# Optimization experiments

Measured on AMD Instinct MI355X. Metric: run time of the kernel, lower is better.

Reference implementation:

```python
import jax, jax.numpy as jnp
import numpy as np

B, S, H = 2, 2048, 2048
NH, KVH, HD = 16, 4, 128
R = 16
LORA_SCALE = 32.0 / 16.0  # lora_alpha / lora_r
ATTN_SCALE = HD ** -0.5
NEG = -1e9


def setup_inputs() -> dict:
    key = jax.random.key(0)
    ks = jax.random.split(key, 16)
    q_dim, kv_dim = NH * HD, KVH * HD
    # RoPE tables
    inv_freq = 1.0 / (10000.0 ** (jnp.arange(0, HD, 2, dtype=jnp.float32) / HD))
    ang = jnp.arange(S, dtype=jnp.float32)[:, None] * inv_freq[None, :]  # [S, HD/2]
    emb = jnp.concatenate([ang, ang], axis=-1)  # [S, HD]
    cos = jnp.broadcast_to(jnp.cos(emb)[None], (B, S, HD))
    sin = jnp.broadcast_to(jnp.sin(emb)[None], (B, S, HD))
    # additive causal mask [B,1,S,S]
    causal = jnp.triu(jnp.full((S, S), NEG, dtype=jnp.float32), k=1)
    attention_mask = jnp.broadcast_to(causal[None, None], (B, 1, S, S))
    return {
        'hidden_states': jax.random.normal(ks[0], (B, S, H), jnp.float32),
        'cos': cos,
        'sin': sin,
        'attention_mask': attention_mask,
        'q_w': jax.random.normal(ks[1], (q_dim, H), jnp.float32) * 0.02,
        'k_w': jax.random.normal(ks[2], (kv_dim, H), jnp.float32) * 0.02,
        'v_w': jax.random.normal(ks[3], (kv_dim, H), jnp.float32) * 0.02,
        'q_b': jax.random.normal(ks[4], (q_dim,), jnp.float32) * 0.02,
        'k_b': jax.random.normal(ks[5], (kv_dim,), jnp.float32) * 0.02,
        'v_b': jax.random.normal(ks[6], (kv_dim,), jnp.float32) * 0.02,
        'q_A': jax.random.normal(ks[7], (H, R), jnp.float32) * (1.0 / np.sqrt(H)),
        'q_B': jax.random.normal(ks[8], (R, q_dim), jnp.float32) * 0.02,
        'k_A': jax.random.normal(ks[9], (H, R), jnp.float32) * (1.0 / np.sqrt(H)),
        'k_B': jax.random.normal(ks[10], (R, kv_dim), jnp.float32) * 0.02,
        'v_A': jax.random.normal(ks[11], (H, R), jnp.float32) * (1.0 / np.sqrt(H)),
        'v_B': jax.random.normal(ks[12], (R, kv_dim), jnp.float32) * 0.02,
        'o_w': jax.random.normal(ks[13], (H, H), jnp.float32) * 0.02,
    }


def _rotate_half(x):
    x1, x2 = x[..., : HD // 2], x[..., HD // 2:]
    return jnp.concatenate([-x2, x1], axis=-1)


def reference(hidden_states, cos, sin, attention_mask,
              q_w, k_w, v_w, q_b, k_b, v_b,
              q_A, q_B, k_A, k_B, v_A, v_B, o_w):
    x = hidden_states  # dropout p=0 (eval)
    # fused base + LoRA projections
    q = x @ q_w.T + q_b + LORA_SCALE * ((x @ q_A) @ q_B)  # [B,S,NH*HD]
    k = x @ k_w.T + k_b + LORA_SCALE * ((x @ k_A) @ k_B)  # [B,S,KVH*HD]
    v = x @ v_w.T + v_b + LORA_SCALE * ((x @ v_A) @ v_B)
    q = q.reshape(B, S, NH, HD).transpose(0, 2, 1, 3)   # [B,NH,S,HD]
    k = k.reshape(B, S, KVH, HD).transpose(0, 2, 1, 3)  # [B,KVH,S,HD]
    v = v.reshape(B, S, KVH, HD).transpose(0, 2, 1, 3)
    # RoPE
    c = cos[:, None]  # [B,1,S,HD]
    s = sin[:, None]
    q = q * c + _rotate_half(q) * s
    k = k * c + _rotate_half(k) * s
    # GQA: repeat kv heads
    n_rep = NH // KVH
    k = jnp.repeat(k, n_rep, axis=1)  # [B,NH,S,HD]
    v = jnp.repeat(v, n_rep, axis=1)
    scores = jnp.einsum('bhqd,bhkd->bhqk', q, k) * ATTN_SCALE
    scores = scores + attention_mask
    attn = jax.nn.softmax(scores.astype(jnp.float32), axis=-1).astype(q.dtype)
    out = jnp.einsum('bhqk,bhkd->bhqd', attn, v)
    out = out.transpose(0, 2, 1, 3).reshape(B, S, NH * HD)  # [B,S,H]
    return out @ o_w.T
```

## Files before the change

### kernel.cpp

```cpp
#include <hip/hip_runtime.h>

constexpr int cB   = 2;
constexpr int cS   = 2048;
constexpr int cH   = 2048;
constexpr int cNH  = 16;
constexpr int cKVH = 4;
constexpr int cHD  = 128;
constexpr int cQD  = 2048;
constexpr int cKVD = 512;
constexpr int cNQKV = 3072;
constexpr int cNTOK = 4096;
#define ATTN_SCALE 0.08838834764831845f

typedef __bf16 bf16;
typedef __attribute__((ext_vector_type(8))) __bf16 bf16x8;
typedef __attribute__((ext_vector_type(4))) __bf16 bf16x4;
typedef __attribute__((ext_vector_type(4))) float  f32x4;

__device__ __forceinline__ void async_load16(const bf16* g, bf16* l) {
    __builtin_amdgcn_global_load_lds(
        (const __attribute__((address_space(1))) void*)g,
        (__attribute__((address_space(3))) void*)l, 16, 0, 0);
}

__global__ void conv_f32_bf16(const float* __restrict__ in, bf16* __restrict__ out) {
    int i = (blockIdx.x * 256 + threadIdx.x) * 4;
    f32x4 v = *(const f32x4*)(in + i);
    bf16x4 o;
    o[0] = (bf16)v[0]; o[1] = (bf16)v[1]; o[2] = (bf16)v[2]; o[3] = (bf16)v[3];
    *(bf16x4*)(out + i) = o;
}

__global__ void prep_w(const float* __restrict__ qw, const float* __restrict__ kw, const float* __restrict__ vw,
                       const float* __restrict__ qA, const float* __restrict__ qB,
                       const float* __restrict__ kA, const float* __restrict__ kB,
                       const float* __restrict__ vA, const float* __restrict__ vB,
                       bf16* __restrict__ Wc) {
    const int idx = blockIdx.x * 256 + threadIdx.x;
    const int n = idx >> 11, k = idx & 2047;
    const float* W; const float* Am; const float* Bm; int nn, nd;
    if (n < cQD)             { W = qw; Am = qA; Bm = qB; nn = n;          nd = cQD; }
    else if (n < cQD + cKVD) { W = kw; Am = kA; Bm = kB; nn = n - cQD;    nd = cKVD; }
    else                     { W = vw; Am = vA; Bm = vB; nn = n - cQD - cKVD; nd = cKVD; }
    float acc = 0.f;
    #pragma unroll
    for (int r = 0; r < 16; ++r) acc += Am[k * 16 + r] * Bm[r * nd + nn];
    Wc[(size_t)n * cH + k] = (bf16)(W[(size_t)nn * cH + k] + 2.0f * acc);
}

__global__ void prep_bias(const float* __restrict__ qb, const float* __restrict__ kb,
                          const float* __restrict__ vb, float* __restrict__ biasc) {
    int n = blockIdx.x * 256 + threadIdx.x;
    if (n >= cNQKV) return;
    biasc[n] = (n < cQD) ? qb[n] : (n < cQD + cKVD ? kb[n - cQD] : vb[n - cQD - cKVD]);
}

__global__ __launch_bounds__(256) void gemm_qkv(const bf16* __restrict__ A, const bf16* __restrict__ Bw,
                                                const float* __restrict__ bias,
                                                const float* __restrict__ cosb, const float* __restrict__ sinb,
                                                bf16* __restrict__ Qr, bf16* __restrict__ Kr,
                                                bf16* __restrict__ Vt) {
    __shared__ bf16 Al[128 * 32];
    __shared__ bf16 Bl[128 * 32];
    const int tid = threadIdx.x;
    const int wave = tid >> 6, lane = tid & 63;
    const int quad = lane >> 4, l16 = lane & 15;
    const int wr = wave >> 1, wc = wave & 1;
    const long bm = (long)blockIdx.y * 128, bn = (long)blockIdx.x * 128;
    const int K = cH;

    f32x4 acc[4][4];
    #pragma unroll
    for (int i = 0; i < 4; ++i)
        #pragma unroll
        for (int c = 0; c < 4; ++c) acc[i][c] = f32x4{0.f, 0.f, 0.f, 0.f};

    const int r0 = lane >> 2;
    const int kc = (lane & 3) * 8;

    for (int k0 = 0; k0 < K; k0 += 32) {
        __syncthreads();
        #pragma unroll
        for (int j = 0; j < 2; ++j) {
            const int rb = (wave * 2 + j) * 16;
            const int row = rb + r0;
            async_load16(A  + (size_t)(bm + row) * K + k0 + kc, &Al[rb * 32 + r0 * 32 + kc]);
            async_load16(Bw + (size_t)(bn + row) * K + k0 + kc, &Bl[rb * 32 + r0 * 32 + kc]);
        }
        __syncthreads();
        bf16x8 af[4], bfr[4];
        #pragma unroll
        for (int i = 0; i < 4; ++i) af[i]  = *(const bf16x8*)&Al[(wr * 64 + i * 16 + l16) * 32 + quad * 8];
        #pragma unroll
        for (int c = 0; c < 4; ++c) {
            const int nrow = wc * 32 + (c & 1) * 16 + (c >> 1) * 64 + l16;
            bfr[c] = *(const bf16x8*)&Bl[nrow * 32 + quad * 8];
        }
        #pragma unroll
        for (int i = 0; i < 4; ++i)
            #pragma unroll
            for (int c = 0; c < 4; ++c)
                acc[i][c] = __builtin_amdgcn_mfma_f32_16x16x32_bf16(af[i], bfr[c], acc[i][c], 0, 0, 0);
    }

    #pragma unroll
    for (int c = 0; c < 4; ++c) {
        const int nloc = wc * 32 + (c & 1) * 16 + (c >> 1) * 64 + l16;
        const float bv = bias[bn + nloc];
        #pragma unroll
        for (int i = 0; i < 4; ++i)
            #pragma unroll
            for (int r = 0; r < 4; ++r) acc[i][c][r] += bv;
    }

    const int head = (int)(bn >> 7);
    if (head < cNH + cKVH) {
        const bool isQ = head < cNH;
        #pragma unroll
        for (int cl = 0; cl < 2; ++cl) {
            const int d = wc * 32 + cl * 16 + l16;
            #pragma unroll
            for (int i = 0; i < 4; ++i)
                #pragma unroll
                for (int r = 0; r < 4; ++r) {
                    const long t = bm + wr * 64 + i * 16 + quad * 4 + r;
                    const float cv = cosb[t * cHD + d];
                    const float sv = sinb[t * cHD + d];
                    const float v1 = acc[i][cl][r], v2 = acc[i][cl + 2][r];
                    float o1 = v1 * cv - v2 * sv;
                    float o2 = v2 * cv + v1 * sv;
                    if (isQ) { o1 *= ATTN_SCALE; o2 *= ATTN_SCALE; }
                    const int b = (int)(t >> 11), s = (int)(t & 2047);
                    bf16* dst = isQ
                        ? Qr + ((size_t)(b * cNH + head) * cS + s) * cHD
                        : Kr + ((size_t)(b * cKVH + (head - cNH)) * cS + s) * cHD;
                    dst[d]      = (bf16)o1;
                    dst[d + 64] = (bf16)o2;
                }
        }
    } else {
        const int kv = head - cNH - cKVH;
        const int b = (int)(bm >> 11);
        const int sbase = (int)(bm & 2047);
        #pragma unroll
        for (int c = 0; c < 4; ++c) {
            const int d = wc * 32 + (c & 1) * 16 + (c >> 1) * 64 + l16;
            #pragma unroll
            for (int i = 0; i < 4; ++i) {
                const int s0 = sbase + wr * 64 + i * 16 + quad * 4;
                bf16x4 o4;
                #pragma unroll
                for (int r = 0; r < 4; ++r) o4[r] = (bf16)acc[i][c][r];
                *(bf16x4*)&Vt[((size_t)((b * cKVH + kv) * cHD) + d) * cS + s0] = o4;
            }
        }
    }
}

__global__ __launch_bounds__(256) void gemm_bt_f32(const bf16* __restrict__ A, const bf16* __restrict__ Bw,
                                                   float* __restrict__ Cp, int M, int N, int K) {
    __shared__ bf16 Al[128 * 32];
    __shared__ bf16 Bl[128 * 32];
    const int tid = threadIdx.x;
    const int wave = tid >> 6, lane = tid & 63;
    const int quad = lane >> 4, l16 = lane & 15;
    const int wr = wave >> 1, wc = wave & 1;
    const long bm = (long)blockIdx.y * 128, bn = (long)blockIdx.x * 128;

    f32x4 acc[4][4];
    #pragma unroll
    for (int i = 0; i < 4; ++i)
        #pragma unroll
        for (int c = 0; c < 4; ++c) acc[i][c] = f32x4{0.f, 0.f, 0.f, 0.f};

    const int r0 = lane >> 2;
    const int kc = (lane & 3) * 8;

    for (int k0 = 0; k0 < K; k0 += 32) {
        __syncthreads();
        #pragma unroll
        for (int j = 0; j < 2; ++j) {
            const int rb = (wave * 2 + j) * 16;
            const int row = rb + r0;
            async_load16(A  + (size_t)(bm + row) * K + k0 + kc, &Al[rb * 32 + r0 * 32 + kc]);
            async_load16(Bw + (size_t)(bn + row) * K + k0 + kc, &Bl[rb * 32 + r0 * 32 + kc]);
        }
        __syncthreads();
        bf16x8 af[4], bfr[4];
        #pragma unroll
        for (int i = 0; i < 4; ++i) af[i]  = *(const bf16x8*)&Al[(wr * 64 + i * 16 + l16) * 32 + quad * 8];
        #pragma unroll
        for (int c = 0; c < 4; ++c) bfr[c] = *(const bf16x8*)&Bl[(wc * 64 + c * 16 + l16) * 32 + quad * 8];
        #pragma unroll
        for (int i = 0; i < 4; ++i)
            #pragma unroll
            for (int c = 0; c < 4; ++c)
                acc[i][c] = __builtin_amdgcn_mfma_f32_16x16x32_bf16(af[i], bfr[c], acc[i][c], 0, 0, 0);
    }

    #pragma unroll
    for (int i = 0; i < 4; ++i)
        #pragma unroll
        for (int c = 0; c < 4; ++c) {
            const long m0 = bm + wr * 64 + i * 16 + quad * 4;
            const long n  = bn + wc * 64 + c * 16 + l16;
            #pragma unroll
            for (int r = 0; r < 4; ++r)
                Cp[(m0 + r) * N + n] = acc[i][c][r];
        }
}

__global__ __launch_bounds__(256, 2) void flash4(const bf16* __restrict__ Q, const bf16* __restrict__ K,
                                                 const bf16* __restrict__ Vt, bf16* __restrict__ Ob) {
    __shared__ bf16 kb[8192];
    __shared__ bf16 vb[8192];
    __shared__ bf16 pb[4096];
    const int tid = threadIdx.x;
    const int wave = tid >> 6, lane = tid & 63;
    const int quad = lane >> 4, l16 = lane & 15;
    const int pi = blockIdx.x;
    const int h = blockIdx.y, b = blockIdx.z;

    const bf16* Qh = Q  + (size_t)(b * cNH + h) * cS * cHD;
    const bf16* Kg = K  + (size_t)(b * cKVH + (h >> 2)) * cS * cHD;
    const bf16* Vg = Vt + (size_t)(b * cKVH + (h >> 2)) * cHD * cS;

    int kgo[4], vgo[4], slo[4];
    #pragma unroll
    for (int i2 = 0; i2 < 4; ++i2) {
        const int si = i2 * 256 + tid;
        const int krow = si >> 4, kcsw = si & 15;
        const int kc = (kcsw & 8) | ((kcsw & 7) ^ (krow & 7));
        kgo[i2] = krow * cHD + kc * 8;
        const int vrow = si >> 3, vcsw = si & 7;
        const int vc = vcsw ^ (vrow & 7);
        vgo[i2] = vrow * cS + vc * 8;
        slo[i2] = si * 8;
    }

    #pragma unroll
    for (int t2 = 0; t2 < 2; ++t2) {
        const int qt = t2 == 0 ? (31 - pi) : pi;

        const bf16* Qg = Qh + (size_t)qt * 64 * cHD;
        bf16x8 qf[4];
        #pragma unroll
        for (int ks = 0; ks < 4; ++ks)
            qf[ks] = *(const bf16x8*)(Qg + (size_t)(wave * 16 + l16) * cHD + ks * 32 + quad * 8);

        f32x4 oac[8];
        #pragma unroll
        for (int dt = 0; dt < 8; ++dt) oac[dt] = f32x4{0.f, 0.f, 0.f, 0.f};
        float m_ = -3.0e38f, l_ = 0.f;

        const int nkt = qt + 1;
        for (int kt = 0; kt < nkt; ++kt) {
            __syncthreads();
            const bf16* Kt  = Kg + (size_t)kt * 64 * cHD;
            const bf16* Vtt = Vg + kt * 64;
            #pragma unroll
            for (int i2 = 0; i2 < 4; ++i2) async_load16(Kt + kgo[i2], kb + slo[i2]);
            #pragma unroll
            for (int i2 = 0; i2 < 4; ++i2) async_load16(Vtt + vgo[i2], vb + slo[i2]);
            __syncthreads();

            f32x4 st[4];
            #pragma unroll
            for (int mt = 0; mt < 4; ++mt) {
                bf16x8 kf[4];
                #pragma unroll
                for (int ks = 0; ks < 4; ++ks) {
                    const int c = ks * 4 + quad;
                    const int csw = (c & 8) | ((c & 7) ^ (l16 & 7));
                    kf[ks] = *(const bf16x8*)&kb[(mt * 16 + l16) * 128 + csw * 8];
                }
                f32x4 a = f32x4{0.f, 0.f, 0.f, 0.f};
                #pragma unroll
                for (int ks = 0; ks < 4; ++ks)
                    a = __builtin_amdgcn_mfma_f32_16x16x32_bf16(kf[ks], qf[ks], a, 0, 0, 0);
                st[mt] = a;
            }

            const int qpos = qt * 64 + wave * 16 + l16;
            const bool dm = (kt * 64 + 63) > (qt * 64 + wave * 16);
            float tmax = -3.0e38f;
            #pragma unroll
            for (int mt = 0; mt < 4; ++mt)
                #pragma unroll
                for (int r = 0; r < 4; ++r) {
                    float v = st[mt][r];
                    if (dm) {
                        const int kpos = kt * 64 + mt * 16 + quad * 4 + r;
                        if (kpos > qpos) v = -3.0e38f;
                    }
                    st[mt][r] = v;
                    tmax = fmaxf(tmax, v);
                }
            tmax = fmaxf(tmax, __shfl_xor(tmax, 16, 64));
            tmax = fmaxf(tmax, __shfl_xor(tmax, 32, 64));
            const float mnew = fmaxf(m_, tmax);
            const float alpha = __expf(m_ - mnew);
            m_ = mnew;
            float rs = 0.f;
            #pragma unroll
            for (int mt = 0; mt < 4; ++mt)
                #pragma unroll
                for (int r = 0; r < 4; ++r) {
                    const float p = __expf(st[mt][r] - mnew);
                    st[mt][r] = p;
                    rs += p;
                }
            rs += __shfl_xor(rs, 16, 64);
            rs += __shfl_xor(rs, 32, 64);
            l_ = l_ * alpha + rs;
            #pragma unroll
            for (int dt = 0; dt < 8; ++dt)
                #pragma unroll
                for (int r = 0; r < 4; ++r) oac[dt][r] *= alpha;

            #pragma unroll
            for (int mt = 0; mt < 4; ++mt) {
                bf16x4 p4;
                #pragma unroll
                for (int r = 0; r < 4; ++r) p4[r] = (bf16)st[mt][r];
                const int csw = (mt * 2 + (quad >> 1)) ^ (l16 & 7);
                *(bf16x4*)&pb[wave * 1024 + l16 * 64 + csw * 8 + (quad & 1) * 4] = p4;
            }

            bf16x8 pf[2];
            #pragma unroll
            for (int ks = 0; ks < 2; ++ks) {
                const int c = ks * 4 + quad;
                const int csw = c ^ (l16 & 7);
                pf[ks] = *(const bf16x8*)&pb[wave * 1024 + l16 * 64 + csw * 8];
            }
            #pragma unroll
            for (int dt = 0; dt < 8; ++dt) {
                bf16x8 vf[2];
                #pragma unroll
                for (int ks = 0; ks < 2; ++ks) {
                    const int c = ks * 4 + quad;
                    const int csw = c ^ (l16 & 7);
                    vf[ks] = *(const bf16x8*)&vb[(dt * 16 + l16) * 64 + csw * 8];
                }
                #pragma unroll
                for (int ks = 0; ks < 2; ++ks)
                    oac[dt] = __builtin_amdgcn_mfma_f32_16x16x32_bf16(vf[ks], pf[ks], oac[dt], 0, 0, 0);
            }
        }

        const float inv = 1.0f / l_;
        const int token = qt * 64 + wave * 16 + l16;
        bf16* orow = Ob + (size_t)(b * cS + token) * (cNH * cHD) + h * cHD;
        #pragma unroll
        for (int dt = 0; dt < 8; ++dt) {
            bf16x4 o4;
            #pragma unroll
            for (int r = 0; r < 4; ++r) o4[r] = (bf16)(oac[dt][r] * inv);
            *(bf16x4*)&orow[dt * 16 + quad * 4] = o4;
        }
    }
}

extern "C" void kernel_launch(void* const* d_in, const int* in_sizes, int n_in,
                              void* d_out, int out_size, void* d_ws, size_t ws_size,
                              hipStream_t stream) {
    const float* x    = (const float*)d_in[0];
    const float* cosb = (const float*)d_in[1];
    const float* sinb = (const float*)d_in[2];
    const float* qw = (const float*)d_in[4];
    const float* kw = (const float*)d_in[5];
    const float* vw = (const float*)d_in[6];
    const float* qb = (const float*)d_in[7];
    const float* kb_ = (const float*)d_in[8];
    const float* vb = (const float*)d_in[9];
    const float* qA = (const float*)d_in[10];
    const float* qB = (const float*)d_in[11];
    const float* kA = (const float*)d_in[12];
    const float* kB = (const float*)d_in[13];
    const float* vA = (const float*)d_in[14];
    const float* vB = (const float*)d_in[15];
    const float* ow = (const float*)d_in[16];
    float* out = (float*)d_out;

    char* ws = (char*)d_ws;
    bf16* Xbf   = (bf16*)ws;  ws += (size_t)cNTOK * cH * 2;
    bf16* Wc    = (bf16*)ws;  ws += (size_t)cNQKV * cH * 2;
    float* biasc = (float*)ws; ws += (size_t)cNQKV * 4;
    bf16* Qr    = (bf16*)ws;  ws += (size_t)cB * cNH * cS * cHD * 2;
    bf16* Kr    = (bf16*)ws;  ws += (size_t)cB * cKVH * cS * cHD * 2;
    bf16* Vt    = (bf16*)ws;  ws += (size_t)cB * cKVH * cHD * cS * 2;
    bf16* OWbf  = (bf16*)ws;  ws += (size_t)cH * cH * 2;
    bf16* Aout  = (bf16*)ws;  ws += (size_t)cNTOK * cQD * 2;

    conv_f32_bf16<<<(cNTOK * cH) / 1024, 256, 0, stream>>>(x, Xbf);
    conv_f32_bf16<<<(cH * cH) / 1024, 256, 0, stream>>>(ow, OWbf);
    prep_w<<<(cNQKV * cH) / 256, 256, 0, stream>>>(qw, kw, vw, qA, qB, kA, kB, vA, vB, Wc);
    prep_bias<<<(cNQKV + 255) / 256, 256, 0, stream>>>(qb, kb_, vb, biasc);

    gemm_qkv<<<dim3(cNQKV / 128, cNTOK / 128), 256, 0, stream>>>(Xbf, Wc, biasc, cosb, sinb, Qr, Kr, Vt);

    flash4<<<dim3(16, cNH, cB), 256, 0, stream>>>(Qr, Kr, Vt, Aout);

    gemm_bt_f32<<<dim3(cH / 128, cNTOK / 128), 256, 0, stream>>>(Aout, OWbf, out, cNTOK, cH, cH);
}
```

Measured before the change: 406.8 us.

## Widen GEMM K-tile with swizzled LDS, vectorize weight prep, use exp2 in flash softmax

Both GEMMs now stage 64-wide K tiles into LDS with an XOR swizzle, which halves the number of loop iterations and barriers and avoids LDS bank conflicts. Weight prep is rewritten to handle 8 contiguous K elements per thread with vector loads, and the bias-prep kernel is folded into it. The flash kernel folds log2(e) into the Q scale so softmax can use exp2. It also skips the accumulator rescale when no row max increases and splits the masked and unmasked max paths. Doubling LDS per block may lower occupancy.

```diff
diff --git a/kernel.cpp b/kernel.cpp
--- a/kernel.cpp
+++ b/kernel.cpp
@@ -11,6 +11,7 @@
 constexpr int cNQKV = 3072;
 constexpr int cNTOK = 4096;
 #define ATTN_SCALE 0.08838834764831845f
+#define QSCALE 0.12751589549581288f
 
 typedef __bf16 bf16;
 typedef __attribute__((ext_vector_type(8))) __bf16 bf16x8;
@@ -31,28 +32,40 @@
     *(bf16x4*)(out + i) = o;
 }
 
-__global__ void prep_w(const float* __restrict__ qw, const float* __restrict__ kw, const float* __restrict__ vw,
-                       const float* __restrict__ qA, const float* __restrict__ qB,
-                       const float* __restrict__ kA, const float* __restrict__ kB,
-                       const float* __restrict__ vA, const float* __restrict__ vB,
-                       bf16* __restrict__ Wc) {
-    const int idx = blockIdx.x * 256 + threadIdx.x;
-    const int n = idx >> 11, k = idx & 2047;
-    const float* W; const float* Am; const float* Bm; int nn, nd;
-    if (n < cQD)             { W = qw; Am = qA; Bm = qB; nn = n;          nd = cQD; }
-    else if (n < cQD + cKVD) { W = kw; Am = kA; Bm = kB; nn = n - cQD;    nd = cKVD; }
-    else                     { W = vw; Am = vA; Bm = vB; nn = n - cQD - cKVD; nd = cKVD; }
-    float acc = 0.f;
-    #pragma unroll
-    for (int r = 0; r < 16; ++r) acc += Am[k * 16 + r] * Bm[r * nd + nn];
-    Wc[(size_t)n * cH + k] = (bf16)(W[(size_t)nn * cH + k] + 2.0f * acc);
-}
-
-__global__ void prep_bias(const float* __restrict__ qb, const float* __restrict__ kb,
-                          const float* __restrict__ vb, float* __restrict__ biasc) {
-    int n = blockIdx.x * 256 + threadIdx.x;
-    if (n >= cNQKV) return;
-    biasc[n] = (n < cQD) ? qb[n] : (n < cQD + cKVD ? kb[n - cQD] : vb[n - cQD - cKVD]);
+__global__ __launch_bounds__(256) void prep_w2(
+        const float* __restrict__ qw, const float* __restrict__ kw, const float* __restrict__ vw,
+        const float* __restrict__ qA, const float* __restrict__ qB,
+        const float* __restrict__ kA, const float* __restrict__ kB,
+        const float* __restrict__ vA, const float* __restrict__ vB,
+        const float* __restrict__ qb, const float* __restrict__ kbias, const float* __restrict__ vb,
+        bf16* __restrict__ Wc, float* __restrict__ biasc) {
+    const int wave = threadIdx.x >> 6, lane = threadIdx.x & 63;
+    const int n = blockIdx.y * 4 + wave;
+    const int k0 = blockIdx.x * 512 + lane * 8;
+    const float* W; const float* Am; const float* Bm; const float* bias; int nn, nd;
+    if (n < cQD)             { W = qw; Am = qA; Bm = qB; bias = qb;    nn = n;               nd = cQD; }
+    else if (n < cQD + cKVD) { W = kw; Am = kA; Bm = kB; bias = kbias; nn = n - cQD;         nd = cKVD; }
+    else                     { W = vw; Am = vA; Bm = vB; bias = vb;    nn = n - cQD - cKVD;  nd = cKVD; }
+    if (blockIdx.x == 0 && lane == 0) biasc[n] = bias[nn];
+    float bm[16];
+    #pragma unroll
+    for (int r = 0; r < 16; ++r) bm[r] = Bm[r * nd + nn];
+    const float* wrow = W + (size_t)nn * cH + k0;
+    f32x4 w0 = *(const f32x4*)(wrow);
+    f32x4 w1 = *(const f32x4*)(wrow + 4);
+    bf16x8 o;
+    #pragma unroll
+    for (int j = 0; j < 8; ++j) {
+        const f32x4* am = (const f32x4*)(Am + (size_t)(k0 + j) * 16);
+        f32x4 a0 = am[0], a1 = am[1], a2 = am[2], a3 = am[3];
+        float acc = 0.f;
+        #pragma unroll
+        for (int c = 0; c < 4; ++c) acc += a0[c] * bm[c] + a1[c] * bm[4 + c]
+                                         + a2[c] * bm[8 + c] + a3[c] * bm[12 + c];
+        const float wv = (j < 4) ? w0[j] : w1[j - 4];
+        o[j] = (bf16)(wv + 2.0f * acc);
+    }
+    *(bf16x8*)&Wc[(size_t)n * cH + k0] = o;
 }
 
 __global__ __launch_bounds__(256) void gemm_qkv(const bf16* __restrict__ A, const bf16* __restrict__ Bw,
@@ -60,8 +73,8 @@
                                                 const float* __restrict__ cosb, const float* __restrict__ sinb,
                                                 bf16* __restrict__ Qr, bf16* __restrict__ Kr,
                                                 bf16* __restrict__ Vt) {
-    __shared__ bf16 Al[128 * 32];
-    __shared__ bf16 Bl[128 * 32];
+    __shared__ bf16 Al[128 * 64];
+    __shared__ bf16 Bl[128 * 64];
     const int tid = threadIdx.x;
     const int wave = tid >> 6, lane = tid & 63;
     const int quad = lane >> 4, l16 = lane & 15;
@@ -75,32 +88,44 @@
         #pragma unroll
         for (int c = 0; c < 4; ++c) acc[i][c] = f32x4{0.f, 0.f, 0.f, 0.f};
 
-    const int r0 = lane >> 2;
-    const int kc = (lane & 3) * 8;
-
-    for (int k0 = 0; k0 < K; k0 += 32) {
+    int ago[4], slo[4];
+    #pragma unroll
+    for (int i2 = 0; i2 < 4; ++i2) {
+        const int si = i2 * 256 + tid;
+        const int row = si >> 3, c8 = si & 7;
+        const int csw = c8 ^ (row & 7);
+        ago[i2] = row * K + csw * 8;
+        slo[i2] = si * 8;
+    }
+    const size_t bmK = (size_t)bm * K, bnK = (size_t)bn * K;
+    const int sw = l16 & 7;
+
+    for (int k0 = 0; k0 < K; k0 += 64) {
         __syncthreads();
         #pragma unroll
-        for (int j = 0; j < 2; ++j) {
-            const int rb = (wave * 2 + j) * 16;
-            const int row = rb + r0;
-            async_load16(A  + (size_t)(bm + row) * K + k0 + kc, &Al[rb * 32 + r0 * 32 + kc]);
-            async_load16(Bw + (size_t)(bn + row) * K + k0 + kc, &Bl[rb * 32 + r0 * 32 + kc]);
-        }
+        for (int i2 = 0; i2 < 4; ++i2) async_load16(A  + bmK + k0 + ago[i2], Al + slo[i2]);
+        #pragma unroll
+        for (int i2 = 0; i2 < 4; ++i2) async_load16(Bw + bnK + k0 + ago[i2], Bl + slo[i2]);
         __syncthreads();
-        bf16x8 af[4], bfr[4];
-        #pragma unroll
-        for (int i = 0; i < 4; ++i) af[i]  = *(const bf16x8*)&Al[(wr * 64 + i * 16 + l16) * 32 + quad * 8];
-        #pragma unroll
-        for (int c = 0; c < 4; ++c) {
-            const int nrow = wc * 32 + (c & 1) * 16 + (c >> 1) * 64 + l16;
-            bfr[c] = *(const bf16x8*)&Bl[nrow * 32 + quad * 8];
-        }
-        #pragma unroll
-        for (int i = 0; i < 4; ++i)
-            #pragma unroll
-            for (int c = 0; c < 4; ++c)
-                acc[i][c] = __builtin_amdgcn_mfma_f32_16x16x32_bf16(af[i], bfr[c], acc[i][c], 0, 0, 0);
+        #pragma unroll
+        for (int ks = 0; ks < 2; ++ks) {
+            const int g = ks * 4 + quad;
+            const int cofs = (g ^ sw) * 8;
+            bf16x8 af[4], bfr[4];
+            #pragma unroll
+            for (int i = 0; i < 4; ++i)
+                af[i] = *(const bf16x8*)&Al[(wr * 64 + i * 16 + l16) * 64 + cofs];
+            #pragma unroll
+            for (int c = 0; c < 4; ++c) {
+                const int nrow = wc * 32 + (c & 1) * 16 + (c >> 1) * 64 + l16;
+                bfr[c] = *(const bf16x8*)&Bl[nrow * 64 + cofs];
+            }
+            #pragma unroll
+            for (int i = 0; i < 4; ++i)
+                #pragma unroll
+                for (int c = 0; c < 4; ++c)
+                    acc[i][c] = __builtin_amdgcn_mfma_f32_16x16x32_bf16(af[i], bfr[c], acc[i][c], 0, 0, 0);
+        }
     }
 
     #pragma unroll
@@ -129,7 +154,7 @@
                     const float v1 = acc[i][cl][r], v2 = acc[i][cl + 2][r];
                     float o1 = v1 * cv - v2 * sv;
                     float o2 = v2 * cv + v1 * sv;
-                    if (isQ) { o1 *= ATTN_SCALE; o2 *= ATTN_SCALE; }
+                    if (isQ) { o1 *= QSCALE; o2 *= QSCALE; }
                     const int b = (int)(t >> 11), s = (int)(t & 2047);
                     bf16* dst = isQ
                         ? Qr + ((size_t)(b * cNH + head) * cS + s) * cHD
@@ -159,8 +184,8 @@
 
 __global__ __launch_bounds__(256) void gemm_bt_f32(const bf16* __restrict__ A, const bf16* __restrict__ Bw,
                                                    float* __restrict__ Cp, int M, int N, int K) {
-    __shared__ bf16 Al[128 * 32];
-    __shared__ bf16 Bl[128 * 32];
+    __shared__ bf16 Al[128 * 64];
+    __shared__ bf16 Bl[128 * 64];
     const int tid = threadIdx.x;
     const int wave = tid >> 6, lane = tid & 63;
     const int quad = lane >> 4, l16 = lane & 15;
@@ -173,29 +198,41 @@
         #pragma unroll
         for (int c = 0; c < 4; ++c) acc[i][c] = f32x4{0.f, 0.f, 0.f, 0.f};
 
-    const int r0 = lane >> 2;
-    const int kc = (lane & 3) * 8;
-
-    for (int k0 = 0; k0 < K; k0 += 32) {
+    int ago[4], slo[4];
+    #pragma unroll
+    for (int i2 = 0; i2 < 4; ++i2) {
+        const int si = i2 * 256 + tid;
+        const int row = si >> 3, c8 = si & 7;
+        const int csw = c8 ^ (row & 7);
+        ago[i2] = row * K + csw * 8;
+        slo[i2] = si * 8;
+    }
+    const size_t bmK = (size_t)bm * K, bnK = (size_t)bn * K;
+    const int sw = l16 & 7;
+
+    for (int k0 = 0; k0 < K; k0 += 64) {
         __syncthreads();
         #pragma unroll
-        for (int j = 0; j < 2; ++j) {
-            const int rb = (wave * 2 + j) * 16;
-            const int row = rb + r0;
-            async_load16(A  + (size_t)(bm + row) * K + k0 + kc, &Al[rb * 32 + r0 * 32 + kc]);
-            async_load16(Bw + (size_t)(bn + row) * K + k0 + kc, &Bl[rb * 32 + r0 * 32 + kc]);
-        }
+        for (int i2 = 0; i2 < 4; ++i2) async_load16(A  + bmK + k0 + ago[i2], Al + slo[i2]);
+        #pragma unroll
+        for (int i2 = 0; i2 < 4; ++i2) async_load16(Bw + bnK + k0 + ago[i2], Bl + slo[i2]);
         __syncthreads();
-        bf16x8 af[4], bfr[4];
-        #pragma unroll
-        for (int i = 0; i < 4; ++i) af[i]  = *(const bf16x8*)&Al[(wr * 64 + i * 16 + l16) * 32 + quad * 8];
-        #pragma unroll
-        for (int c = 0; c < 4; ++c) bfr[c] = *(const bf16x8*)&Bl[(wc * 64 + c * 16 + l16) * 32 + quad * 8];
-        #pragma unroll
-        for (int i = 0; i < 4; ++i)
+        #pragma unroll
+        for (int ks = 0; ks < 2; ++ks) {
+            const int cofs = ((ks * 4 + quad) ^ sw) * 8;
+            bf16x8 af[4], bfr[4];
+            #pragma unroll
+            for (int i = 0; i < 4; ++i)
+                af[i] = *(const bf16x8*)&Al[(wr * 64 + i * 16 + l16) * 64 + cofs];
             #pragma unroll
             for (int c = 0; c < 4; ++c)
-                acc[i][c] = __builtin_amdgcn_mfma_f32_16x16x32_bf16(af[i], bfr[c], acc[i][c], 0, 0, 0);
+                bfr[c] = *(const bf16x8*)&Bl[(wc * 64 + c * 16 + l16) * 64 + cofs];
+            #pragma unroll
+            for (int i = 0; i < 4; ++i)
+                #pragma unroll
+                for (int c = 0; c < 4; ++c)
+                    acc[i][c] = __builtin_amdgcn_mfma_f32_16x16x32_bf16(af[i], bfr[c], acc[i][c], 0, 0, 0);
+        }
     }
 
     #pragma unroll
@@ -282,41 +319,46 @@
             }
 
             const int qpos = qt * 64 + wave * 16 + l16;
-            const bool dm = (kt * 64 + 63) > (qt * 64 + wave * 16);
             float tmax = -3.0e38f;
-            #pragma unroll
-            for (int mt = 0; mt < 4; ++mt)
-                #pragma unroll
-                for (int r = 0; r < 4; ++r) {
-                    float v = st[mt][r];
-                    if (dm) {
+            if ((kt * 64 + 63) > (qt * 64 + wave * 16)) {
+                #pragma unroll
+                for (int mt = 0; mt < 4; ++mt)
+                    #pragma unroll
+                    for (int r = 0; r < 4; ++r) {
                         const int kpos = kt * 64 + mt * 16 + quad * 4 + r;
-                        if (kpos > qpos) v = -3.0e38f;
+                        if (kpos > qpos) st[mt][r] = -3.0e38f;
+                        tmax = fmaxf(tmax, st[mt][r]);
                     }
-                    st[mt][r] = v;
-                    tmax = fmaxf(tmax, v);
-                }
+            } else {
+                #pragma unroll
+                for (int mt = 0; mt < 4; ++mt)
+                    #pragma unroll
+                    for (int r = 0; r < 4; ++r) tmax = fmaxf(tmax, st[mt][r]);
+            }
             tmax = fmaxf(tmax, __shfl_xor(tmax, 16, 64));
             tmax = fmaxf(tmax, __shfl_xor(tmax, 32, 64));
             const float mnew = fmaxf(m_, tmax);
-            const float alpha = __expf(m_ - mnew);
+            if (__any(tmax > m_)) {
+                const float alpha = __builtin_amdgcn_exp2f(m_ - mnew);
+                l_ *= alpha;
+                #pragma unroll
+                for (int dt = 0; dt < 8; ++dt)
+                    #pragma unroll
+                    for (int r = 0; r < 4; ++r) oac[dt][r] *= alpha;
+            }
             m_ = mnew;
             float rs = 0.f;
             #pragma unroll
             for (int mt = 0; mt < 4; ++mt)
                 #pragma unroll
                 for (int r = 0; r < 4; ++r) {
-                    const float p = __expf(st[mt][r] - mnew);
+                    const float p = __builtin_amdgcn_exp2f(st[mt][r] - mnew);
                     st[mt][r] = p;
                     rs += p;
                 }
             rs += __shfl_xor(rs, 16, 64);
             rs += __shfl_xor(rs, 32, 64);
-            l_ = l_ * alpha + rs;
-            #pragma unroll
-            for (int dt = 0; dt < 8; ++dt)
-                #pragma unroll
-                for (int r = 0; r < 4; ++r) oac[dt][r] *= alpha;
+            l_ += rs;
 
             #pragma unroll
             for (int mt = 0; mt < 4; ++mt) {
@@ -395,8 +437,8 @@
 
     conv_f32_bf16<<<(cNTOK * cH) / 1024, 256, 0, stream>>>(x, Xbf);
     conv_f32_bf16<<<(cH * cH) / 1024, 256, 0, stream>>>(ow, OWbf);
-    prep_w<<<(cNQKV * cH) / 256, 256, 0, stream>>>(qw, kw, vw, qA, qB, kA, kB, vA, vB, Wc);
-    prep_bias<<<(cNQKV + 255) / 256, 256, 0, stream>>>(qb, kb_, vb, biasc);
+    prep_w2<<<dim3(cH / 512, cNQKV / 4), 256, 0, stream>>>(qw, kw, vw, qA, qB, kA, kB, vA, vB,
+                                                           qb, kb_, vb, Wc, biasc);
 
     gemm_qkv<<<dim3(cNQKV / 128, cNTOK / 128), 256, 0, stream>>>(Xbf, Wc, biasc, cosb, sinb, Qr, Kr, Vt);
 
```

Result: faster. 395.3 us (-2.8%).
